# Kernel optimization log

Hardware: AMD Instinct MI355X
Metric: run time of the kernel (lower is better)

Reference implementation:

```python
import jax, jax.numpy as jnp
import numpy as np

IN_FEATURES = 4096
OUT_FEATURES = 4096
WBITS = 4
GROUPSIZE = 128
PACK_FACTOR = 32 // WBITS  # 8
MASK = (1 << WBITS) - 1    # 15


def setup_inputs() -> dict:
    key = jax.random.key(0)
    k1, k2, k3, k4, k5 = jax.random.split(key, 5)
    x = jax.random.normal(k1, (4, 2048, IN_FEATURES), dtype=jnp.float32)
    # Packed 4-bit weights: (in_features*wbits//32, out_features) int32 words.
    qweight = jax.random.randint(k2, (IN_FEATURES * WBITS // 32, OUT_FEATURES),
                                 jnp.iinfo(jnp.int32).min, jnp.iinfo(jnp.int32).max,
                                 dtype=jnp.int32)
    num_groups = IN_FEATURES // GROUPSIZE  # 32
    # Packed zero points: (num_groups, out_features*wbits//32) int32 words.
    qzeros = jax.random.randint(k3, (num_groups, OUT_FEATURES * WBITS // 32),
                                jnp.iinfo(jnp.int32).min, jnp.iinfo(jnp.int32).max,
                                dtype=jnp.int32)
    scales = jax.random.uniform(k4, (num_groups, OUT_FEATURES), dtype=jnp.float32,
                                minval=0.001, maxval=0.02)
    bias = jax.random.normal(k5, (OUT_FEATURES,), dtype=jnp.float32)
    return {"x": x, "qweight": qweight, "qzeros": qzeros, "scales": scales, "bias": bias}


def _unpack4(packed, axis_len):
    """Unpack int32 words along a new inner axis of PACK_FACTOR 4-bit nibbles.

    packed: (..., n_words) -> (..., n_words*PACK_FACTOR) int32 in [0, 15].
    """
    shifts = (jnp.arange(PACK_FACTOR, dtype=jnp.int32) * WBITS)
    nib = (packed[..., :, None] >> shifts) & MASK  # (..., n_words, PACK_FACTOR)
    return nib.reshape(*packed.shape[:-1], axis_len)


def reference(x, qweight, qzeros, scales, bias):
    # Unpack weights: qweight is packed along in_features (dim 0).
    # (in/8, 8, out) -> (in, out) int nibbles.
    shifts = (jnp.arange(PACK_FACTOR, dtype=jnp.int32) * WBITS)
    wq = ((qweight[:, None, :] >> shifts[None, :, None]) & MASK)
    wq = wq.reshape(IN_FEATURES, OUT_FEATURES)  # [in, out] int32 in [0,15]
    # Unpack zeros: packed along out_features (dim 1); AutoGPTQ stores zero-1,
    # so add 1 back at dequant time.
    zq = _unpack4(qzeros, OUT_FEATURES) + 1  # [num_groups, out]
    g_idx = jnp.arange(IN_FEATURES, dtype=jnp.int32) // GROUPSIZE  # [in]
    # Per-group affine dequant: W[i,o] = s[g(i),o] * (wq[i,o] - z[g(i),o])
    W = scales[g_idx] * (wq - zq[g_idx]).astype(scales.dtype)  # [in, out]
    # y = x @ W + b  (x: [b, s, in])
    return jnp.einsum('bsi,io->bso', x, W) + bias
```

## Files before the change

### kernel.cpp

```cpp
#include <hip/hip_runtime.h>
#include <hip/hip_bf16.h>
#include <stdint.h>


#define M_TOT 8192
#define N_TOT 4096
#define K_TOT 4096
#define NT    (K_TOT / 64)

using bf16x8 = __attribute__((ext_vector_type(8))) __bf16;
using f32x4  = __attribute__((ext_vector_type(4))) float;

__device__ __forceinline__ unsigned short f2bf(float f) {
  unsigned u = __builtin_bit_cast(unsigned, f);
  u += 0x7fffu + ((u >> 16) & 1u);
  return (unsigned short)(u >> 16);
}

__global__ void cvt_x_kernel(const float* __restrict__ x,
                             unsigned short* __restrict__ xb, int n) {
  int stride = gridDim.x * blockDim.x * 8;
  for (int i = (blockIdx.x * blockDim.x + threadIdx.x) * 8; i < n; i += stride) {
    float4 a = *reinterpret_cast<const float4*>(x + i);
    float4 b = *reinterpret_cast<const float4*>(x + i + 4);
    unsigned short o[8] = {f2bf(a.x), f2bf(a.y), f2bf(a.z), f2bf(a.w),
                           f2bf(b.x), f2bf(b.y), f2bf(b.z), f2bf(b.w)};
    *reinterpret_cast<uint4*>(xb + i) = *reinterpret_cast<const uint4*>(o);
  }
}

__global__ void dequant_wt_kernel(const int* __restrict__ qweight,
                                  const int* __restrict__ qzeros,
                                  const float* __restrict__ scales,
                                  unsigned short* __restrict__ wt) {
  int t = blockIdx.x * blockDim.x + threadIdx.x;
  int nn = t >> 9;
  int kw = t & 511;
  int g  = kw >> 4;
  unsigned w = (unsigned)qweight[kw * N_TOT + nn];
  float s = scales[g * N_TOT + nn];
  unsigned zw = (unsigned)qzeros[g * (N_TOT / 8) + (nn >> 3)];
  float z = (float)(((zw >> ((nn & 7) * 4)) & 15u) + 1u);
  unsigned short o[8];
#pragma unroll
  for (int j = 0; j < 8; ++j) {
    float v = s * ((float)((w >> (4 * j)) & 15u) - z);
    o[j] = f2bf(v);
  }
  *reinterpret_cast<uint4*>(wt + (size_t)nn * K_TOT + kw * 8) =
      *reinterpret_cast<const uint4*>(o);
}

__device__ __forceinline__ void gll16(const unsigned short* g, const unsigned short* l) {
  __builtin_amdgcn_global_load_lds(
      (const __attribute__((address_space(1))) void*)(uintptr_t)g,
      (__attribute__((address_space(3))) void*)(uintptr_t)l, 16, 0, 0);
}

__global__ __launch_bounds__(512, 2) void gemm_8phase_kernel(
    const unsigned short* __restrict__ A,
    const unsigned short* __restrict__ B,
    const float* __restrict__ bias,
    float* __restrict__ C) {
  __shared__ __align__(16) unsigned short As[2 * 256 * 64];
  __shared__ __align__(16) unsigned short Bs[2 * 256 * 64];

  int bid = blockIdx.x;
  int swz = (bid & 7) * 64 + (bid >> 3);
  int bm = swz & 31, bn = swz >> 5;
  int m0 = bm * 256, n0 = bn * 256;

  int t = threadIdx.x;
  int lane = t & 63;
  int wave = t >> 6;
  int wr = wave >> 2, wc = wave & 3;
  int lr = lane & 15, kq = lane >> 4;

  int rowL0 = t >> 3;
  int jlog  = ((t & 7) ^ (rowL0 & 7)) * 8;
  const unsigned short* aG = A + (size_t)(m0 + rowL0) * K_TOT + jlog;
  const unsigned short* bG = B + (size_t)(n0 + rowL0) * K_TOT + jlog;

  unsigned rbA = (unsigned)((wr * 128 + lr) * 128 + ((kq * 16) ^ ((lr & 7) << 4)));
  unsigned rbB = (unsigned)((wc * 64  + lr) * 128 + ((kq * 16) ^ ((lr & 7) << 4)));

  f32x4 acc[8][4] = {};

#define STAGE(matG, ldsArr, tile, h)                                              \
  do {                                                                            \
    const unsigned short* _g = (matG) + (size_t)(h) * 128 * K_TOT +               \
                               (size_t)(tile) * 64;                               \
    const unsigned short* _l = (ldsArr) + ((tile) & 1) * 16384 + (h) * 8192 +     \
                               t * 8;                                             \
    gll16(_g, _l);                                                                \
    gll16(_g + (size_t)64 * K_TOT, _l + 4096);                                    \
  } while (0)

  STAGE(aG, As, 0, 0);
  STAGE(aG, As, 0, 1);
  STAGE(bG, Bs, 0, 0);
  STAGE(bG, Bs, 0, 1);
  STAGE(bG, Bs, 1, 0);
  STAGE(bG, Bs, 1, 1);
  asm volatile("s_waitcnt vmcnt(4)" ::: "memory");
  __builtin_amdgcn_s_barrier();

  for (int tt = 0; tt < NT; ++tt) {
    const char* aBuf = (const char*)As + (tt & 1) * 32768;
    const char* bBuf = (const char*)Bs + (tt & 1) * 32768;
    bf16x8 bh[4][2];

#pragma unroll
    for (int q = 0; q < 4; ++q) {
      if (q == 0) {
#pragma unroll
        for (int n = 0; n < 4; ++n)
#pragma unroll
          for (int s = 0; s < 2; ++s)
            bh[n][s] = *(const bf16x8*)(bBuf + ((rbB + n * 2048) ^ (s * 64)));
      }
      bf16x8 a0[2][2];
#pragma unroll
      for (int mm = 0; mm < 2; ++mm)
#pragma unroll
        for (int s = 0; s < 2; ++s)
          a0[mm][s] = *(const bf16x8*)(aBuf + ((rbA + (2 * q + mm) * 2048) ^ (s * 64)));

      if (q == 0 && tt + 1 < NT) STAGE(aG, As, tt + 1, 0);
      if (q == 1 && tt + 1 < NT) STAGE(aG, As, tt + 1, 1);
      if (q == 1 && tt + 2 < NT) STAGE(bG, Bs, tt + 2, 0);
      if (q == 2 && tt + 2 < NT) STAGE(bG, Bs, tt + 2, 1);

      __builtin_amdgcn_s_barrier();
      __builtin_amdgcn_s_setprio(1);
#pragma unroll
      for (int s = 0; s < 2; ++s)
#pragma unroll
        for (int mm = 0; mm < 2; ++mm)
#pragma unroll
          for (int n = 0; n < 4; ++n)
            acc[2 * q + mm][n] = __builtin_amdgcn_mfma_f32_16x16x32_bf16(
                a0[mm][s], bh[n][s], acc[2 * q + mm][n], 0, 0, 0);
      __builtin_amdgcn_s_setprio(0);
      if (q == 3) {
        if (tt >= NT - 2) asm volatile("s_waitcnt vmcnt(0)" ::: "memory");
        else              asm volatile("s_waitcnt vmcnt(4)" ::: "memory");
      }
      __builtin_amdgcn_s_barrier();
    }
  }
#undef STAGE

#pragma unroll
  for (int n = 0; n < 4; ++n) {
    int ncol = n0 + wc * 64 + n * 16 + lr;
    float bz = bias[ncol];
#pragma unroll
    for (int m = 0; m < 8; ++m) {
      int mrow = m0 + wr * 128 + m * 16 + kq * 4;
#pragma unroll
      for (int r = 0; r < 4; ++r)
        C[(size_t)(mrow + r) * N_TOT + ncol] = acc[m][n][r] + bz;
    }
  }
}

extern "C" void kernel_launch(void* const* d_in, const int* in_sizes, int n_in,
                              void* d_out, int out_size, void* d_ws, size_t ws_size,
                              hipStream_t stream) {
  const float* x       = (const float*)d_in[0];
  const int*   qweight = (const int*)d_in[1];
  const int*   qzeros  = (const int*)d_in[2];
  const float* scales  = (const float*)d_in[3];
  const float* bias    = (const float*)d_in[4];
  float* out = (float*)d_out;

  const size_t xb_bytes = (size_t)M_TOT * K_TOT * 2;
  const size_t wt_bytes = (size_t)N_TOT * K_TOT * 2;
  if (ws_size < xb_bytes + wt_bytes) return;

  unsigned short* Xb = (unsigned short*)d_ws;
  unsigned short* Wt = (unsigned short*)((char*)d_ws + xb_bytes);

  cvt_x_kernel<<<2048, 256, 0, stream>>>(x, Xb, M_TOT * K_TOT);
  dequant_wt_kernel<<<(N_TOT * 512) / 256, 256, 0, stream>>>(qweight, qzeros, scales, Wt);

  dim3 grid((M_TOT / 256) * (N_TOT / 256));
  gemm_8phase_kernel<<<grid, 512, 0, stream>>>(Xb, Wt, bias, out);
}
```

Baseline: 296.9 us.

## Software-pipeline LDS fragment loads ahead of MFMAs and reschedule global staging

Double-buffers the A register fragments so that the next quarter's LDS reads are issued right after the current MFMA block. The next tile's B and first A fragments are preloaded before the loop and at the end of each iteration. Global-to-LDS staging moves to later phases and the barrier count per iteration is reduced. The aim is to hide LDS read latency behind MFMA work. In exchange it uses more registers and needs subtler barrier and vmcnt ordering, which puts correctness and occupancy at risk.

```diff
diff --git a/kernel.cpp b/kernel.cpp
--- a/kernel.cpp
+++ b/kernel.cpp
@@ -85,6 +85,8 @@
   unsigned rbB = (unsigned)((wc * 64  + lr) * 128 + ((kq * 16) ^ ((lr & 7) << 4)));
 
   f32x4 acc[8][4] = {};
+  bf16x8 av[2][2][2];
+  bf16x8 bh[4][2];
 
 #define STAGE(matG, ldsArr, tile, h)                                              \
   do {                                                                            \
@@ -104,34 +106,31 @@
   STAGE(bG, Bs, 1, 1);
   asm volatile("s_waitcnt vmcnt(4)" ::: "memory");
   __builtin_amdgcn_s_barrier();
-
+  __builtin_amdgcn_sched_barrier(0);
+
+  {
+    const char* aB0 = (const char*)As;
+    const char* bB0 = (const char*)Bs;
+#pragma unroll
+    for (int n = 0; n < 4; ++n)
+#pragma unroll
+      for (int s = 0; s < 2; ++s)
+        bh[n][s] = *(const bf16x8*)(bB0 + ((rbB + n * 2048) ^ (s * 64)));
+#pragma unroll
+    for (int mm = 0; mm < 2; ++mm)
+#pragma unroll
+      for (int s = 0; s < 2; ++s)
+        av[0][mm][s] = *(const bf16x8*)(aB0 + ((rbA + mm * 2048) ^ (s * 64)));
+  }
+
+#pragma unroll 2
   for (int tt = 0; tt < NT; ++tt) {
     const char* aBuf = (const char*)As + (tt & 1) * 32768;
-    const char* bBuf = (const char*)Bs + (tt & 1) * 32768;
-    bf16x8 bh[4][2];
 
 #pragma unroll
     for (int q = 0; q < 4; ++q) {
-      if (q == 0) {
-#pragma unroll
-        for (int n = 0; n < 4; ++n)
-#pragma unroll
-          for (int s = 0; s < 2; ++s)
-            bh[n][s] = *(const bf16x8*)(bBuf + ((rbB + n * 2048) ^ (s * 64)));
-      }
-      bf16x8 a0[2][2];
-#pragma unroll
-      for (int mm = 0; mm < 2; ++mm)
-#pragma unroll
-        for (int s = 0; s < 2; ++s)
-          a0[mm][s] = *(const bf16x8*)(aBuf + ((rbA + (2 * q + mm) * 2048) ^ (s * 64)));
-
-      if (q == 0 && tt + 1 < NT) STAGE(aG, As, tt + 1, 0);
-      if (q == 1 && tt + 1 < NT) STAGE(aG, As, tt + 1, 1);
-      if (q == 1 && tt + 2 < NT) STAGE(bG, Bs, tt + 2, 0);
-      if (q == 2 && tt + 2 < NT) STAGE(bG, Bs, tt + 2, 1);
-
-      __builtin_amdgcn_s_barrier();
+      if (q) __builtin_amdgcn_s_barrier();
+
       __builtin_amdgcn_s_setprio(1);
 #pragma unroll
       for (int s = 0; s < 2; ++s)
@@ -140,13 +139,44 @@
 #pragma unroll
           for (int n = 0; n < 4; ++n)
             acc[2 * q + mm][n] = __builtin_amdgcn_mfma_f32_16x16x32_bf16(
-                a0[mm][s], bh[n][s], acc[2 * q + mm][n], 0, 0, 0);
+                av[q & 1][mm][s], bh[n][s], acc[2 * q + mm][n], 0, 0, 0);
       __builtin_amdgcn_s_setprio(0);
+
+      if (q < 3) {
+#pragma unroll
+        for (int mm = 0; mm < 2; ++mm)
+#pragma unroll
+          for (int s = 0; s < 2; ++s)
+            av[(q + 1) & 1][mm][s] = *(const bf16x8*)(
+                aBuf + ((rbA + (2 * (q + 1) + mm) * 2048) ^ (s * 64)));
+      }
+
+      if (q == 1 && tt + 1 < NT) STAGE(aG, As, tt + 1, 0);
+      if (q == 2) {
+        if (tt + 1 < NT) STAGE(aG, As, tt + 1, 1);
+        if (tt + 2 < NT) STAGE(bG, Bs, tt + 2, 0);
+      }
       if (q == 3) {
-        if (tt >= NT - 2) asm volatile("s_waitcnt vmcnt(0)" ::: "memory");
+        if (tt + 2 < NT) STAGE(bG, Bs, tt + 2, 1);
+        if (tt >= NT - 3) asm volatile("s_waitcnt vmcnt(0)" ::: "memory");
         else              asm volatile("s_waitcnt vmcnt(4)" ::: "memory");
+        __builtin_amdgcn_s_barrier();
+        __builtin_amdgcn_sched_barrier(0);
+        if (tt + 1 < NT) {
+          const char* aN = (const char*)As + ((tt + 1) & 1) * 32768;
+          const char* bN = (const char*)Bs + ((tt + 1) & 1) * 32768;
+#pragma unroll
+          for (int n = 0; n < 4; ++n)
+#pragma unroll
+            for (int s = 0; s < 2; ++s)
+              bh[n][s] = *(const bf16x8*)(bN + ((rbB + n * 2048) ^ (s * 64)));
+#pragma unroll
+          for (int mm = 0; mm < 2; ++mm)
+#pragma unroll
+            for (int s = 0; s < 2; ++s)
+              av[0][mm][s] = *(const bf16x8*)(aN + ((rbA + mm * 2048) ^ (s * 64)));
+        }
       }
-      __builtin_amdgcn_s_barrier();
     }
   }
 #undef STAGE
```

Result: faster. 287.8 us (-3.0%).

## Restructure GEMM main loop into two K-halves with register double-buffering

Applied to the files above, without the earlier changes.

Replaces the four-phase per-tile loop with a K-split schedule. Each 64-wide K tile is processed as two 32-wide halves, and the fragments for one half are loaded into registers while the other half's MFMAs run. Global-to-LDS prefetch of both A and B for tile tt+2 is now issued together at the end of each iteration, and the loop is unrolled by two. The aim is fewer barriers and better overlap of LDS reads with MFMA. The cost is more register pressure, and a full vmcnt(0) wait mid-iteration that leaves only about half a tile of compute to hide global load latency.

```diff
diff --git a/kernel.cpp b/kernel.cpp
--- a/kernel.cpp
+++ b/kernel.cpp
@@ -57,7 +57,7 @@
       (__attribute__((address_space(3))) void*)(uintptr_t)l, 16, 0, 0);
 }
 
-__global__ __launch_bounds__(512, 2) void gemm_8phase_kernel(
+__global__ __launch_bounds__(512, 2) void gemm_ksplit_kernel(
     const unsigned short* __restrict__ A,
     const unsigned short* __restrict__ B,
     const float* __restrict__ bias,
@@ -85,6 +85,7 @@
   unsigned rbB = (unsigned)((wc * 64  + lr) * 128 + ((kq * 16) ^ ((lr & 7) << 4)));
 
   f32x4 acc[8][4] = {};
+  bf16x8 avA[8], bhA[4], avB[8], bhB[4];
 
 #define STAGE(matG, ldsArr, tile, h)                                              \
   do {                                                                            \
@@ -100,54 +101,76 @@
   STAGE(aG, As, 0, 1);
   STAGE(bG, Bs, 0, 0);
   STAGE(bG, Bs, 0, 1);
+  STAGE(aG, As, 1, 0);
+  STAGE(aG, As, 1, 1);
   STAGE(bG, Bs, 1, 0);
   STAGE(bG, Bs, 1, 1);
-  asm volatile("s_waitcnt vmcnt(4)" ::: "memory");
+  asm volatile("s_waitcnt vmcnt(8)" ::: "memory");
   __builtin_amdgcn_s_barrier();
-
+  __builtin_amdgcn_sched_barrier(0);
+
+#pragma unroll
+  for (int m = 0; m < 8; ++m)
+    avA[m] = *(const bf16x8*)((const char*)As + (rbA + m * 2048));
+#pragma unroll
+  for (int n = 0; n < 4; ++n)
+    bhA[n] = *(const bf16x8*)((const char*)Bs + (rbB + n * 2048));
+
+#pragma unroll 2
   for (int tt = 0; tt < NT; ++tt) {
-    const char* aBuf = (const char*)As + (tt & 1) * 32768;
-    const char* bBuf = (const char*)Bs + (tt & 1) * 32768;
-    bf16x8 bh[4][2];
-
-#pragma unroll
-    for (int q = 0; q < 4; ++q) {
-      if (q == 0) {
-#pragma unroll
-        for (int n = 0; n < 4; ++n)
-#pragma unroll
-          for (int s = 0; s < 2; ++s)
-            bh[n][s] = *(const bf16x8*)(bBuf + ((rbB + n * 2048) ^ (s * 64)));
-      }
-      bf16x8 a0[2][2];
-#pragma unroll
-      for (int mm = 0; mm < 2; ++mm)
-#pragma unroll
-        for (int s = 0; s < 2; ++s)
-          a0[mm][s] = *(const bf16x8*)(aBuf + ((rbA + (2 * q + mm) * 2048) ^ (s * 64)));
-
-      if (q == 0 && tt + 1 < NT) STAGE(aG, As, tt + 1, 0);
-      if (q == 1 && tt + 1 < NT) STAGE(aG, As, tt + 1, 1);
-      if (q == 1 && tt + 2 < NT) STAGE(bG, Bs, tt + 2, 0);
-      if (q == 2 && tt + 2 < NT) STAGE(bG, Bs, tt + 2, 1);
-
-      __builtin_amdgcn_s_barrier();
-      __builtin_amdgcn_s_setprio(1);
-#pragma unroll
-      for (int s = 0; s < 2; ++s)
-#pragma unroll
-        for (int mm = 0; mm < 2; ++mm)
-#pragma unroll
-          for (int n = 0; n < 4; ++n)
-            acc[2 * q + mm][n] = __builtin_amdgcn_mfma_f32_16x16x32_bf16(
-                a0[mm][s], bh[n][s], acc[2 * q + mm][n], 0, 0, 0);
-      __builtin_amdgcn_s_setprio(0);
-      if (q == 3) {
-        if (tt >= NT - 2) asm volatile("s_waitcnt vmcnt(0)" ::: "memory");
-        else              asm volatile("s_waitcnt vmcnt(4)" ::: "memory");
-      }
-      __builtin_amdgcn_s_barrier();
+    const char* aBuf  = (const char*)As + (tt & 1) * 32768;
+    const char* bBuf  = (const char*)Bs + (tt & 1) * 32768;
+    const char* aNext = (const char*)As + ((tt + 1) & 1) * 32768;
+    const char* bNext = (const char*)Bs + ((tt + 1) & 1) * 32768;
+
+#pragma unroll
+    for (int m = 0; m < 8; ++m)
+      avB[m] = *(const bf16x8*)(aBuf + ((rbA + m * 2048) ^ 64));
+#pragma unroll
+    for (int n = 0; n < 4; ++n)
+      bhB[n] = *(const bf16x8*)(bBuf + ((rbB + n * 2048) ^ 64));
+    __builtin_amdgcn_sched_barrier(0);
+
+    __builtin_amdgcn_s_setprio(1);
+#pragma unroll
+    for (int m = 0; m < 8; ++m)
+#pragma unroll
+      for (int n = 0; n < 4; ++n)
+        acc[m][n] = __builtin_amdgcn_mfma_f32_16x16x32_bf16(
+            avA[m], bhA[n], acc[m][n], 0, 0, 0);
+    __builtin_amdgcn_s_setprio(0);
+
+    asm volatile("s_waitcnt vmcnt(0)" ::: "memory");
+    asm volatile("s_waitcnt lgkmcnt(0)" ::: "memory");
+    __builtin_amdgcn_s_barrier();
+
+    if (tt + 1 < NT) {
+#pragma unroll
+      for (int m = 0; m < 8; ++m)
+        avA[m] = *(const bf16x8*)(aNext + (rbA + m * 2048));
+#pragma unroll
+      for (int n = 0; n < 4; ++n)
+        bhA[n] = *(const bf16x8*)(bNext + (rbB + n * 2048));
     }
+    __builtin_amdgcn_sched_barrier(0);
+
+    __builtin_amdgcn_s_setprio(1);
+#pragma unroll
+    for (int m = 0; m < 8; ++m)
+#pragma unroll
+      for (int n = 0; n < 4; ++n)
+        acc[m][n] = __builtin_amdgcn_mfma_f32_16x16x32_bf16(
+            avB[m], bhB[n], acc[m][n], 0, 0, 0);
+    __builtin_amdgcn_s_setprio(0);
+
+    if (tt + 2 < NT) {
+      STAGE(aG, As, tt + 2, 0);
+      STAGE(aG, As, tt + 2, 1);
+      STAGE(bG, Bs, tt + 2, 0);
+      STAGE(bG, Bs, tt + 2, 1);
+    }
+    asm volatile("s_waitcnt lgkmcnt(0)" ::: "memory");
+    __builtin_amdgcn_s_barrier();
   }
 #undef STAGE
 
@@ -186,5 +209,5 @@
   dequant_wt_kernel<<<(N_TOT * 512) / 256, 256, 0, stream>>>(qweight, qzeros, scales, Wt);
 
   dim3 grid((M_TOT / 256) * (N_TOT / 256));
-  gemm_8phase_kernel<<<grid, 512, 0, stream>>>(Xb, Wt, bias, out);
-}
+  gemm_ksplit_kernel<<<grid, 512, 0, stream>>>(Xb, Wt, bias, out);
+}
```

Result: slower. 878.5 us (+195.9%).

## Restructure GEMM main loop into quadrant phases with register double-buffered LDS reads

Applied to the files above, without the earlier changes.

Replaces the 4-phase per-tile loop with a 4-quadrant schedule (2x2 blocks of 4x2 MFMA tiles). A and B fragments are read from LDS into ping-pong register sets, so the next tile's first fragments load during the last quadrant's MFMAs. The global-to-LDS staging is rebalanced across phases with a deeper A prefetch, and sched_barrier/lgkmcnt fences pin the ordering. This aims to hide LDS read latency behind MFMA work. It costs extra VGPRs under the 2-waves launch bound and makes the staging dependencies fragile.

```diff
diff --git a/kernel.cpp b/kernel.cpp
--- a/kernel.cpp
+++ b/kernel.cpp
@@ -57,7 +57,7 @@
       (__attribute__((address_space(3))) void*)(uintptr_t)l, 16, 0, 0);
 }
 
-__global__ __launch_bounds__(512, 2) void gemm_8phase_kernel(
+__global__ __launch_bounds__(512, 2) void gemm_tmpl_kernel(
     const unsigned short* __restrict__ A,
     const unsigned short* __restrict__ B,
     const float* __restrict__ bias,
@@ -85,6 +85,8 @@
   unsigned rbB = (unsigned)((wc * 64  + lr) * 128 + ((kq * 16) ^ ((lr & 7) << 4)));
 
   f32x4 acc[8][4] = {};
+  bf16x8 avX[4][2], avY[4][2];
+  bf16x8 bhX[2][2], bhY[2][2];
 
 #define STAGE(matG, ldsArr, tile, h)                                              \
   do {                                                                            \
@@ -96,60 +98,99 @@
     gll16(_g + (size_t)64 * K_TOT, _l + 4096);                                    \
   } while (0)
 
+#define READ_A(DST, BUF, MOFF)                                                    \
+  _Pragma("unroll")                                                               \
+  for (int _j = 0; _j < 4; ++_j)                                                  \
+    _Pragma("unroll")                                                             \
+    for (int _s = 0; _s < 2; ++_s)                                                \
+      DST[_j][_s] = *(const bf16x8*)((BUF) +                                      \
+          ((rbA + ((MOFF) + _j) * 2048) ^ (_s * 64)));
+
+#define READ_B(DST, BUF, NOFF)                                                    \
+  _Pragma("unroll")                                                               \
+  for (int _n = 0; _n < 2; ++_n)                                                  \
+    _Pragma("unroll")                                                             \
+    for (int _s = 0; _s < 2; ++_s)                                                \
+      DST[_n][_s] = *(const bf16x8*)((BUF) +                                      \
+          ((rbB + ((NOFF) + _n) * 2048) ^ (_s * 64)));
+
+#define MFMA16(AV, BH, MB, NB)                                                    \
+  _Pragma("unroll")                                                               \
+  for (int _s = 0; _s < 2; ++_s)                                                  \
+    _Pragma("unroll")                                                             \
+    for (int _m = 0; _m < 4; ++_m)                                                \
+      _Pragma("unroll")                                                           \
+      for (int _n = 0; _n < 2; ++_n)                                              \
+        acc[(MB) + _m][(NB) + _n] = __builtin_amdgcn_mfma_f32_16x16x32_bf16(      \
+            AV[_m][_s], BH[_n][_s], acc[(MB) + _m][(NB) + _n], 0, 0, 0);
+
+#define PHASE_SYNC_IN()                                                           \
+  __builtin_amdgcn_sched_barrier(0);                                              \
+  __builtin_amdgcn_s_barrier();                                                   \
+  asm volatile("s_waitcnt lgkmcnt(0)" ::: "memory");                              \
+  __builtin_amdgcn_sched_barrier(0)
+
   STAGE(aG, As, 0, 0);
   STAGE(aG, As, 0, 1);
   STAGE(bG, Bs, 0, 0);
   STAGE(bG, Bs, 0, 1);
+  STAGE(aG, As, 1, 0);
+  STAGE(aG, As, 1, 1);
   STAGE(bG, Bs, 1, 0);
-  STAGE(bG, Bs, 1, 1);
-  asm volatile("s_waitcnt vmcnt(4)" ::: "memory");
+  asm volatile("s_waitcnt vmcnt(6)" ::: "memory");
   __builtin_amdgcn_s_barrier();
-
+  __builtin_amdgcn_sched_barrier(0);
+  READ_A(avX, (const char*)As, 0);
+  READ_B(bhX, (const char*)Bs, 0);
+
+#pragma unroll 2
   for (int tt = 0; tt < NT; ++tt) {
     const char* aBuf = (const char*)As + (tt & 1) * 32768;
     const char* bBuf = (const char*)Bs + (tt & 1) * 32768;
-    bf16x8 bh[4][2];
-
-#pragma unroll
-    for (int q = 0; q < 4; ++q) {
-      if (q == 0) {
-#pragma unroll
-        for (int n = 0; n < 4; ++n)
-#pragma unroll
-          for (int s = 0; s < 2; ++s)
-            bh[n][s] = *(const bf16x8*)(bBuf + ((rbB + n * 2048) ^ (s * 64)));
-      }
-      bf16x8 a0[2][2];
-#pragma unroll
-      for (int mm = 0; mm < 2; ++mm)
-#pragma unroll
-        for (int s = 0; s < 2; ++s)
-          a0[mm][s] = *(const bf16x8*)(aBuf + ((rbA + (2 * q + mm) * 2048) ^ (s * 64)));
-
-      if (q == 0 && tt + 1 < NT) STAGE(aG, As, tt + 1, 0);
-      if (q == 1 && tt + 1 < NT) STAGE(aG, As, tt + 1, 1);
-      if (q == 1 && tt + 2 < NT) STAGE(bG, Bs, tt + 2, 0);
-      if (q == 2 && tt + 2 < NT) STAGE(bG, Bs, tt + 2, 1);
-
-      __builtin_amdgcn_s_barrier();
-      __builtin_amdgcn_s_setprio(1);
-#pragma unroll
-      for (int s = 0; s < 2; ++s)
-#pragma unroll
-        for (int mm = 0; mm < 2; ++mm)
-#pragma unroll
-          for (int n = 0; n < 4; ++n)
-            acc[2 * q + mm][n] = __builtin_amdgcn_mfma_f32_16x16x32_bf16(
-                a0[mm][s], bh[n][s], acc[2 * q + mm][n], 0, 0, 0);
-      __builtin_amdgcn_s_setprio(0);
-      if (q == 3) {
-        if (tt >= NT - 2) asm volatile("s_waitcnt vmcnt(0)" ::: "memory");
-        else              asm volatile("s_waitcnt vmcnt(4)" ::: "memory");
-      }
-      __builtin_amdgcn_s_barrier();
+
+    READ_A(avY, aBuf, 4);
+    READ_B(bhY, bBuf, 2);
+    if (tt + 1 < NT) STAGE(bG, Bs, tt + 1, 1);
+    PHASE_SYNC_IN();
+    __builtin_amdgcn_s_setprio(1);
+    MFMA16(avX, bhX, 0, 0);
+    __builtin_amdgcn_s_setprio(0);
+    __builtin_amdgcn_s_barrier();
+
+    if (tt + 2 < NT) STAGE(aG, As, tt + 2, 0);
+    PHASE_SYNC_IN();
+    __builtin_amdgcn_s_setprio(1);
+    MFMA16(avY, bhX, 4, 0);
+    __builtin_amdgcn_s_setprio(0);
+    __builtin_amdgcn_s_barrier();
+
+    if (tt + 2 < NT) STAGE(aG, As, tt + 2, 1);
+    PHASE_SYNC_IN();
+    __builtin_amdgcn_s_setprio(1);
+    MFMA16(avX, bhY, 0, 2);
+    __builtin_amdgcn_s_setprio(0);
+    if (tt + 2 < NT) asm volatile("s_waitcnt vmcnt(4)" ::: "memory");
+    else             asm volatile("s_waitcnt vmcnt(0)" ::: "memory");
+    __builtin_amdgcn_s_barrier();
+
+    if (tt + 1 < NT) {
+      const char* aN = (const char*)As + ((tt + 1) & 1) * 32768;
+      const char* bN = (const char*)Bs + ((tt + 1) & 1) * 32768;
+      READ_A(avX, aN, 0);
+      READ_B(bhX, bN, 0);
     }
+    if (tt + 2 < NT) STAGE(bG, Bs, tt + 2, 0);
+    PHASE_SYNC_IN();
+    __builtin_amdgcn_s_setprio(1);
+    MFMA16(avY, bhY, 4, 2);
+    __builtin_amdgcn_s_setprio(0);
+    __builtin_amdgcn_s_barrier();
   }
 #undef STAGE
+#undef READ_A
+#undef READ_B
+#undef MFMA16
+#undef PHASE_SYNC_IN
 
 #pragma unroll
   for (int n = 0; n < 4; ++n) {
@@ -186,5 +227,5 @@
   dequant_wt_kernel<<<(N_TOT * 512) / 256, 256, 0, stream>>>(qweight, qzeros, scales, Wt);
 
   dim3 grid((M_TOT / 256) * (N_TOT / 256));
-  gemm_8phase_kernel<<<grid, 512, 0, stream>>>(Xb, Wt, bias, out);
-}
+  gemm_tmpl_kernel<<<grid, 512, 0, stream>>>(Xb, Wt, bias, out);
+}
```

New measurement: 297.6 us. Within noise of the previous version (+0.2%).
